# Optimization experiments

Hardware: AMD Instinct MI355X
Metric: run time of the kernel (lower is better)

Reference implementation:

```python
import jax, jax.numpy as jnp
import numpy as np

B, T, S, H, E, V, NUM_OOV = 32, 32, 100, 512, 300, 45000, 10
INF = 1e12


def setup_inputs() -> dict:
    key = jax.random.key(0)
    ks = jax.random.split(key, 24)
    def n(k, shape, s=0.02):
        return jax.random.normal(k, shape, jnp.float32) * s
    return dict(
        trg_seq=jax.random.randint(ks[0], (B, T), 0, V),
        ext_src_seq=jax.random.randint(ks[1], (B, S), 0, V + NUM_OOV),
        h0=n(ks[2], (1, B, H), 0.1),
        c0=n(ks[3], (1, B, H), 0.1),
        tree_output=n(ks[4], (B, S, H), 1.0),
        tree_enc_states=n(ks[5], (1, B, H), 0.1),
        encoder_outputs=n(ks[6], (B, S, H), 1.0),
        encoder_mask=jnp.zeros((B, S), bool),
        embedding=n(ks[7], (V, E)),
        W_enc=n(ks[8], (2 * H, H)), b_enc=jnp.zeros((H,), jnp.float32),
        W_red=n(ks[9], (E + H, E)), b_red=jnp.zeros((E,), jnp.float32),
        W_ih=n(ks[10], (E, 4 * H)), W_hh=n(ks[11], (H, 4 * H)),
        b_ih=jnp.zeros((4 * H,), jnp.float32), b_hh=jnp.zeros((4 * H,), jnp.float32),
        W_cat=n(ks[12], (2 * H, H)), b_cat=jnp.zeros((H,), jnp.float32),
        W_out=n(ks[13], (H, V)), b_out=jnp.zeros((V,), jnp.float32),
    )


def reference(trg_seq, ext_src_seq, h0, c0, tree_output, tree_enc_states,
              encoder_outputs, encoder_mask, embedding, W_enc, b_enc,
              W_red, b_red, W_ih, W_hh, b_ih, b_hh, W_cat, b_cat, W_out, b_out):
    # encoder features: [B,S,2H] -> [B,S,H]
    memories = jnp.concatenate([tree_output, encoder_outputs], axis=-1) @ W_enc + b_enc
    rows = jnp.arange(B)[:, None]  # for per-row scatter-max
    Vext = V + NUM_OOV

    def step(carry, y):
        h, c, ctx = carry  # h,c: [B,H], ctx: [B,H]
        emb = embedding[y]                                   # [B,E]
        x = jnp.concatenate([emb, ctx], axis=-1) @ W_red + b_red  # [B,E]
        gates = x @ W_ih + h @ W_hh + (b_ih + b_hh)          # [B,4H]
        i, f, g, o = jnp.split(gates, 4, axis=-1)            # torch gate order i,f,g,o
        c_new = jax.nn.sigmoid(f) * c + jax.nn.sigmoid(i) * jnp.tanh(g)
        h_new = jax.nn.sigmoid(o) * jnp.tanh(c_new)
        energy = jnp.einsum('bh,bsh->bs', h_new, memories)   # [B,S]
        energy = jnp.where(encoder_mask, -INF, energy)
        attn = jax.nn.softmax(energy, axis=-1)
        ctx_new = jnp.einsum('bs,bsh->bh', attn, memories)   # [B,H]
        z = jnp.tanh(jnp.concatenate([h_new, ctx_new], axis=-1) @ W_cat + b_cat)
        logit = z @ W_out + b_out                            # [B,V]
        # pointer copy mechanism: scatter-max of energies into extended vocab
        ext = jnp.concatenate([logit, jnp.zeros((B, NUM_OOV), logit.dtype)], axis=-1)
        scat = jnp.full((B, Vext), -INF, logit.dtype).at[rows, ext_src_seq].max(energy)
        scat = jnp.where(scat == -INF, 0.0, scat)
        out = ext + scat
        out = jnp.where(out == 0.0, -INF, out)
        return (h_new, c_new, ctx_new), out

    init = (h0[0], c0[0], jnp.zeros((B, H), memories.dtype))
    _, logits = jax.lax.scan(step, init, trg_seq.T)  # [T,B,Vext]
    return jnp.transpose(logits, (1, 0, 2))          # [B,T,Vext]
```

## Files before the change

### kernel.cpp

```cpp
#include <hip/hip_runtime.h>
#include <hip/hip_bf16.h>
#include <stdint.h>

typedef __hip_bfloat16 bf16;
typedef __attribute__((ext_vector_type(8))) short short8;
typedef __attribute__((ext_vector_type(4))) float f32x4;

#define INFV 1e12f

constexpr int Vv = 45000;
constexpr int VE = 45010;

static __device__ __forceinline__ float bf2f(unsigned short u){
  union{ unsigned int i; float f; } w; w.i = ((unsigned int)u) << 16; return w.f;
}
static __device__ __forceinline__ unsigned short f2bf(float x){
  union { __hip_bfloat16 h; unsigned short u; } w; w.h = __float2bfloat16(x); return w.u;
}

__launch_bounds__(256, 2)
__global__ void k_mm(const unsigned short* __restrict__ A, int lda,
                     const unsigned short* __restrict__ B, int ldb, int NB,
                     const float* __restrict__ bias,
                     void* __restrict__ C, int ldc,
                     int M, int N, int NZ, int K, int mode)
{
  __shared__ char smem[20480];
  char* smA = smem;
  char* smB = smem + 10240;
  int tid = threadIdx.x, lane = tid & 63;
  int w = tid >> 6, wr = w >> 1, wc = w & 1;
  int m0 = blockIdx.y * 128, n0 = blockIdx.x * 128;
  int l15 = lane & 15, lh = lane >> 4;
  f32x4 zero = {0.f,0.f,0.f,0.f};
  f32x4 acc[4][4];
  #pragma unroll
  for (int mi = 0; mi < 4; ++mi)
    #pragma unroll
    for (int ni = 0; ni < 4; ++ni) acc[mi][ni] = zero;
  short8 z8 = {0,0,0,0,0,0,0,0};

  for (int kc = 0; kc < K; kc += 32){
    #pragma unroll
    for (int call = 0; call < 2; ++call){
      int o = call*4096 + tid*16;
      int r = o >> 6, cb = o & 63;
      short8 va = z8, vb = z8;
      if (m0 + r < M)  va = *(const short8*)((const char*)A + ((size_t)(m0+r)*lda + kc)*2 + cb);
      if (n0 + r < NB) vb = *(const short8*)((const char*)B + ((size_t)(n0+r)*ldb + kc)*2 + cb);
      *(short8*)(smA + r*80 + cb) = va;
      *(short8*)(smB + r*80 + cb) = vb;
    }
    __syncthreads();
    short8 af[4], bfv[4];
    #pragma unroll
    for (int mi = 0; mi < 4; ++mi) af[mi]  = *(const short8*)(smA + (wr*64 + mi*16 + l15)*80 + lh*16);
    #pragma unroll
    for (int ni = 0; ni < 4; ++ni) bfv[ni] = *(const short8*)(smB + (wc*64 + ni*16 + l15)*80 + lh*16);
    #pragma unroll
    for (int mi = 0; mi < 4; ++mi)
      #pragma unroll
      for (int ni = 0; ni < 4; ++ni)
        acc[mi][ni] = __builtin_amdgcn_mfma_f32_16x16x32_bf16(af[mi], bfv[ni], acc[mi][ni], 0, 0, 0);
    __syncthreads();
  }

  #pragma unroll
  for (int mi = 0; mi < 4; ++mi){
    #pragma unroll
    for (int ni = 0; ni < 4; ++ni){
      #pragma unroll
      for (int j = 0; j < 4; ++j){
        int gr = m0 + wr*64 + mi*16 + 4*lh + j;
        int cg = n0 + wc*64 + ni*16 + l15;
        if (gr < M && cg < NZ){
          float v = (cg < N) ? acc[mi][ni][j] + (bias ? bias[cg] : 0.f) : 0.f;
          if (mode == 0) ((float*)C)[(size_t)gr*ldc + cg] = v;
          else {
            if (mode == 2) v = tanhf(v);
            ((unsigned short*)C)[(size_t)gr*ldc + cg] = f2bf(v);
          }
        }
      }
    }
  }
}

__launch_bounds__(256)
__global__ void k_tbf(const float* __restrict__ in, int ldin,
                      unsigned short* __restrict__ out,
                      int K, int N, int K2, int N2)
{
  __shared__ float tl[64][65];
  int n0 = blockIdx.x * 64, k0 = blockIdx.y * 64;
  int tid = threadIdx.x;
  for (int idx = tid; idx < 64*64; idx += 256){
    int r = idx >> 6, c = idx & 63;
    int gk = k0 + r, gn = n0 + c;
    tl[r][c] = (gk < K && gn < N) ? in[(size_t)gk*ldin + gn] : 0.f;
  }
  __syncthreads();
  for (int idx = tid; idx < 64*64; idx += 256){
    int r = idx >> 6, c = idx & 63;
    int gn = n0 + r, gk = k0 + c;
    if (gn < N2 && gk < K2) out[(size_t)gn*K2 + gk] = f2bf(tl[c][r]);
  }
}

__global__ void k_cat2bf(const float* __restrict__ tree, const float* __restrict__ enc,
                         unsigned short* __restrict__ Acat){
  int i = blockIdx.x*256 + threadIdx.x;
  if (i >= 3200*1024) return;
  int r = i >> 10, c = i & 1023;
  float v = (c < 512) ? tree[(size_t)r*512 + c] : enc[(size_t)r*512 + (c - 512)];
  Acat[i] = f2bf(v);
}

__global__ void k_gatherbf(const int* __restrict__ trg, const float* __restrict__ emb,
                           unsigned short* __restrict__ EmbAb){
  int i = blockIdx.x*256 + threadIdx.x;
  if (i >= 1024*320) return;
  int r = i / 320, c = i - r*320;
  EmbAb[i] = (c < 300) ? f2bf(emb[(size_t)trg[r]*300 + c]) : (unsigned short)0;
}

__global__ void k_cvtpad(const float* __restrict__ in, unsigned short* __restrict__ out){
  int i = blockIdx.x*256 + threadIdx.x;
  if (i >= 512*320) return;
  int r = i / 320, c = i - r*320;
  out[i] = (c < 300) ? f2bf(in[(size_t)r*300 + c]) : (unsigned short)0;
}

__global__ void k_bsum(const float* __restrict__ a, const float* __restrict__ b,
                       float* __restrict__ o){
  int i = blockIdx.x*256 + threadIdx.x;
  if (i < 2048) o[i] = a[i] + b[i];
}

__global__ void k_wgt(const float* __restrict__ Wf, const float* __restrict__ W_hh,
                      unsigned short* __restrict__ WgT){
  int idx = blockIdx.x*256 + threadIdx.x;
  if (idx >= 2048*1024) return;
  int cp = idx >> 10, k = idx & 1023;
  int c = (cp & 3)*512 + (cp >> 2);
  float v = (k < 512) ? Wf[(size_t)k*2048 + c] : W_hh[(size_t)(k-512)*2048 + c];
  WgT[idx] = f2bf(v);
}

__global__ void k_init(const float* __restrict__ h0, const float* __restrict__ c0,
                       unsigned short* __restrict__ HCa, float* __restrict__ Cst){
  int i = blockIdx.x*256 + threadIdx.x;
  if (i < 32*1024){
    int b = i >> 10, k = i & 1023;
    HCa[i] = (k < 512) ? f2bf(0.f) : f2bf(h0[b*512 + (k - 512)]);
  }
  if (i < 32*512) Cst[i] = c0[i];
}

__launch_bounds__(256, 1)
__global__ void k_gates(const unsigned short* __restrict__ WgT,
                        const unsigned short* __restrict__ HCprev,
                        unsigned short* __restrict__ HCnext,
                        float* __restrict__ C_state,
                        const float* __restrict__ G1,
                        unsigned short* __restrict__ HCz,
                        int t)
{
  __shared__ char Bsm[64*272];
  int tid = threadIdx.x;
  int lane = tid & 63, w2 = tid >> 6;
  int blk = blockIdx.x;
  int l15 = lane & 15, lh = lane >> 4;
  f32x4 zero = {0.f,0.f,0.f,0.f};
  f32x4 acc0 = zero, acc1 = zero;
  const char* Ab = (const char*)HCprev;

  for (int kc = 0; kc < 1024; kc += 128){
    #pragma unroll
    for (int call = 0; call < 4; ++call){
      int o = call*4096 + tid*16;
      int r = o >> 8, cb = o & 255;
      short8 v = *(const short8*)((const char*)WgT + (size_t)(blk*64 + r)*2048 + kc*2 + cb);
      *(short8*)(Bsm + r*272 + cb) = v;
    }
    __syncthreads();
    #pragma unroll
    for (int ks = 0; ks < 4; ++ks){
      short8 a0 = *(const short8*)(Ab + (size_t)l15*2048      + (kc + ks*32)*2 + lh*16);
      short8 a1 = *(const short8*)(Ab + (size_t)(l15+16)*2048 + (kc + ks*32)*2 + lh*16);
      int br = w2*16 + l15;
      short8 bfr = *(const short8*)(Bsm + br*272 + ks*64 + lh*16);
      acc0 = __builtin_amdgcn_mfma_f32_16x16x32_bf16(a0, bfr, acc0, 0, 0, 0);
      acc1 = __builtin_amdgcn_mfma_f32_16x16x32_bf16(a1, bfr, acc1, 0, 0, 0);
    }
    __syncthreads();
  }

  int cg = blk*64 + w2*16 + l15;
  int hfull = cg >> 2, q = cg & 3;
  #pragma unroll
  for (int f = 0; f < 2; ++f){
    #pragma unroll
    for (int j = 0; j < 4; ++j){
      int b = f*16 + 4*lh + j;
      float g = (f ? acc1[j] : acc0[j]) + G1[((size_t)b*32 + t)*2048 + q*512 + hfull];
      float x1 = (q == 2) ? tanhf(g) : 1.f/(1.f + expf(-g));
      float xg = __shfl_xor(x1, 2);
      float xf = __shfl_xor(x1, 1);
      float xo = __shfl_xor(x1, 3);
      if (q == 0){
        float co = C_state[b*512 + hfull];
        float cn = xf*co + x1*xg;
        float hn = xo * tanhf(cn);
        C_state[b*512 + hfull] = cn;
        unsigned short hb = f2bf(hn);
        HCnext[b*1024 + 512 + hfull] = hb;
        HCz[((size_t)b*32 + t)*1024 + hfull] = hb;
      }
    }
  }
}

__launch_bounds__(256, 1)
__global__ void k_attn(const unsigned short* __restrict__ memB,
                       const unsigned char* __restrict__ emask,
                       unsigned short* __restrict__ HCnext,
                       unsigned short* __restrict__ HCz,
                       float* __restrict__ Esave,
                       int t)
{
  int b = blockIdx.x;
  int tid = threadIdx.x, lane = tid & 63, w = tid >> 6;
  __shared__ float E_s[100];
  __shared__ float attn_s[100];
  float hreg[8];
  {
    short8 hv = *(const short8*)(HCnext + b*1024 + 512 + lane*8);
    #pragma unroll
    for (int i = 0; i < 8; ++i) hreg[i] = bf2f((unsigned short)hv[i]);
  }
  for (int s = w; s < 100; s += 4){
    short8 mv = *(const short8*)(memB + ((size_t)b*100 + s)*512 + lane*8);
    float a = 0.f;
    #pragma unroll
    for (int i = 0; i < 8; ++i) a = fmaf(hreg[i], bf2f((unsigned short)mv[i]), a);
    #pragma unroll
    for (int d = 1; d < 64; d <<= 1) a += __shfl_xor(a, d);
    if (lane == 0){
      float e = emask[b*100 + s] ? -INFV : a;
      E_s[s] = e;
      Esave[((size_t)b*32 + t)*100 + s] = e;
    }
  }
  __syncthreads();
  if (w == 0){
    float ea = (lane < 100) ? E_s[lane] : -INFV;
    float eb = (lane + 64 < 100) ? E_s[lane + 64] : -INFV;
    float m = fmaxf(ea, eb);
    #pragma unroll
    for (int d = 1; d < 64; d <<= 1) m = fmaxf(m, __shfl_xor(m, d));
    float p = ((lane < 100) ? expf(ea - m) : 0.f) + ((lane + 64 < 100) ? expf(eb - m) : 0.f);
    #pragma unroll
    for (int d = 1; d < 64; d <<= 1) p += __shfl_xor(p, d);
    float inv = 1.f / p;
    if (lane < 100)      attn_s[lane]      = expf(ea - m) * inv;
    if (lane + 64 < 100) attn_s[lane + 64] = expf(eb - m) * inv;
  }
  __syncthreads();
  for (int hh = tid; hh < 512; hh += 256){
    float a = 0.f;
    for (int s = 0; s < 100; ++s)
      a = fmaf(attn_s[s], bf2f(memB[((size_t)b*100 + s)*512 + hh]), a);
    unsigned short cbv = f2bf(a);
    HCnext[b*1024 + hh] = cbv;
    HCz[((size_t)b*32 + t)*1024 + 512 + hh] = cbv;
  }
}

__launch_bounds__(256, 4)
__global__ void k_logits(const unsigned short* __restrict__ Zbf,
                         const unsigned short* __restrict__ WoT,
                         const float* __restrict__ b_out,
                         const float* __restrict__ Esave,
                         const int* __restrict__ ext_src,
                         float* __restrict__ out)
{
  __shared__ char smem[32768];
  char* smA = smem;
  char* smB = smem + 10240;
  int tid = threadIdx.x, lane = tid & 63;
  int w = tid >> 6, wr = w >> 1, wc = w & 1;
  int m0 = blockIdx.y * 128, n0 = blockIdx.x * 128;
  int l15 = lane & 15, lh = lane >> 4;
  f32x4 zero = {0.f,0.f,0.f,0.f};
  f32x4 acc[4][4];
  #pragma unroll
  for (int mi = 0; mi < 4; ++mi)
    #pragma unroll
    for (int ni = 0; ni < 4; ++ni) acc[mi][ni] = zero;

  for (int kc = 0; kc < 512; kc += 32){
    #pragma unroll
    for (int call = 0; call < 2; ++call){
      int o = call*4096 + tid*16;
      int r = o >> 6, cb = o & 63;
      short8 va = *(const short8*)((const char*)Zbf + (size_t)(m0 + r)*1024 + kc*2 + cb);
      *(short8*)(smA + r*80 + cb) = va;
      short8 vb = *(const short8*)((const char*)WoT + (size_t)(n0 + r)*1024 + kc*2 + cb);
      *(short8*)(smB + r*80 + cb) = vb;
    }
    __syncthreads();
    short8 af[4], bfv[4];
    #pragma unroll
    for (int mi = 0; mi < 4; ++mi) af[mi]  = *(const short8*)(smA + (wr*64 + mi*16 + l15)*80 + lh*16);
    #pragma unroll
    for (int ni = 0; ni < 4; ++ni) bfv[ni] = *(const short8*)(smB + (wc*64 + ni*16 + l15)*80 + lh*16);
    #pragma unroll
    for (int mi = 0; mi < 4; ++mi)
      #pragma unroll
      for (int ni = 0; ni < 4; ++ni)
        acc[mi][ni] = __builtin_amdgcn_mfma_f32_16x16x32_bf16(af[mi], bfv[ni], acc[mi][ni], 0, 0, 0);
    __syncthreads();
  }

  float* smax = (float*)smem;
  for (int half = 0; half < 2; ++half){
    for (int i = tid; i < 64*128; i += 256) smax[i] = -INFV;
    __syncthreads();
    if (tid < 64){
      int rg = m0 + half*64 + tid;
      int b = rg >> 5;
      const int* es = ext_src + b*100;
      const float* ev = Esave + (size_t)rg*100;
      float* row = smax + tid*128;
      for (int s = 0; s < 100; ++s){
        unsigned int d = (unsigned int)(es[s] - n0);
        if (d < 128u){
          float e = ev[s];
          if (e > -9e11f && e > row[d]) row[d] = e;
        }
      }
    }
    __syncthreads();
    if (wr == half){
      #pragma unroll
      for (int mi = 0; mi < 4; ++mi){
        #pragma unroll
        for (int ni = 0; ni < 4; ++ni){
          #pragma unroll
          for (int j = 0; j < 4; ++j){
            int rll = mi*16 + 4*lh + j;
            int cl = wc*64 + ni*16 + l15;
            int cg = n0 + cl;
            if (cg < VE){
              float v = acc[mi][ni][j];
              float base = (cg < Vv) ? (v + b_out[cg]) : 0.f;
              float sm = smax[rll*128 + cl];
              float o = base + (sm > -9e11f ? sm : 0.f);
              if (o == 0.f) o = -INFV;
              out[(size_t)(m0 + half*64 + rll)*VE + cg] = o;
            }
          }
        }
      }
    }
    __syncthreads();
  }
}

extern "C" void kernel_launch(void* const* d_in, const int* in_sizes, int n_in,
                              void* d_out, int out_size, void* d_ws, size_t ws_size,
                              hipStream_t stream)
{
  const int*   trg    = (const int*)  d_in[0];
  const int*   ext    = (const int*)  d_in[1];
  const float* h0     = (const float*)d_in[2];
  const float* c0     = (const float*)d_in[3];
  const float* tree   = (const float*)d_in[4];
  const float* enc    = (const float*)d_in[6];
  const unsigned char* emask = (const unsigned char*)d_in[7];
  const float* emb    = (const float*)d_in[8];
  const float* W_enc  = (const float*)d_in[9];
  const float* b_enc  = (const float*)d_in[10];
  const float* W_red  = (const float*)d_in[11];
  const float* b_red  = (const float*)d_in[12];
  const float* W_ih   = (const float*)d_in[13];
  const float* W_hh   = (const float*)d_in[14];
  const float* b_ih   = (const float*)d_in[15];
  const float* b_hh   = (const float*)d_in[16];
  const float* W_cat  = (const float*)d_in[17];
  const float* b_cat  = (const float*)d_in[18];
  const float* W_out  = (const float*)d_in[19];
  const float* b_out  = (const float*)d_in[20];
  float* out = (float*)d_out;

  char* ws = (char*)d_ws;
  size_t off = 0;
  auto alloc = [&](size_t bytes)->char*{
    char* p = ws + off; off = (off + bytes + 255) & ~(size_t)255; return p;
  };
  unsigned short* Acat  = (unsigned short*)alloc(3200ull*1024*2);
  unsigned short* WencT = (unsigned short*)alloc(512ull*1024*2);
  unsigned short* memB  = (unsigned short*)alloc(3200ull*512*2);
  unsigned short* EmbAb = (unsigned short*)alloc(1024ull*320*2);
  unsigned short* WredT1= (unsigned short*)alloc(320ull*320*2);
  unsigned short* X0b   = (unsigned short*)alloc(1024ull*320*2);
  unsigned short* WihT  = (unsigned short*)alloc(2048ull*320*2);
  float*          G1    = (float*)         alloc(1024ull*2048*4);
  float*          bsum  = (float*)         alloc(2048*4);
  unsigned short* Wred2b= (unsigned short*)alloc(512ull*320*2);
  unsigned short* WgT   = (unsigned short*)alloc(2048ull*1024*2);
  unsigned short* WoT   = (unsigned short*)alloc(45056ull*512*2);
  unsigned short* WcatT = (unsigned short*)alloc(512ull*1024*2);
  unsigned short* HCa   = (unsigned short*)alloc(32*1024*2);
  unsigned short* HCb   = (unsigned short*)alloc(32*1024*2);
  float*          Cst   = (float*)         alloc(32*512*4);
  unsigned short* HCz   = (unsigned short*)alloc(1024ull*1024*2);
  unsigned short* Zbf   = (unsigned short*)alloc(1024ull*512*2);
  float*          Esave = (float*)         alloc(1024ull*100*4);
  float*          Wf    = (float*)Acat;

  k_cat2bf<<<12800, 256, 0, stream>>>(tree, enc, Acat);
  k_tbf<<<dim3(8,16), 256, 0, stream>>>(W_enc, 512, WencT, 1024, 512, 1024, 512);
  k_mm<<<dim3(4,25), 256, 0, stream>>>(Acat, 1024, WencT, 1024, 512, b_enc,
                                       memB, 512, 3200, 512, 512, 1024, 1);

  k_gatherbf<<<1280, 256, 0, stream>>>(trg, emb, EmbAb);
  k_tbf<<<dim3(5,5), 256, 0, stream>>>(W_red, 300, WredT1, 300, 300, 320, 320);
  k_tbf<<<dim3(32,5), 256, 0, stream>>>(W_ih, 2048, WihT, 300, 2048, 320, 2048);
  k_bsum<<<8, 256, 0, stream>>>(b_ih, b_hh, bsum);
  k_mm<<<dim3(3,8), 256, 0, stream>>>(EmbAb, 320, WredT1, 320, 320, b_red,
                                      X0b, 320, 1024, 300, 320, 320, 1);
  k_mm<<<dim3(16,8), 256, 0, stream>>>(X0b, 320, WihT, 320, 2048, bsum,
                                       G1, 2048, 1024, 2048, 2048, 320, 0);

  k_cvtpad<<<640, 256, 0, stream>>>(W_red + 300*300, Wred2b);
  k_mm<<<dim3(16,4), 256, 0, stream>>>(Wred2b, 320, WihT, 320, 2048, nullptr,
                                       Wf, 2048, 512, 2048, 2048, 320, 0);
  k_wgt<<<8192, 256, 0, stream>>>(Wf, W_hh, WgT);

  k_tbf<<<dim3(704,8), 256, 0, stream>>>(W_out, 45000, WoT, 512, 45000, 512, 45056);
  k_tbf<<<dim3(8,16), 256, 0, stream>>>(W_cat, 512, WcatT, 1024, 512, 1024, 512);
  k_init<<<128, 256, 0, stream>>>(h0, c0, HCa, Cst);

  for (int t = 0; t < 32; ++t){
    unsigned short* hp = (t & 1) ? HCb : HCa;
    unsigned short* hn = (t & 1) ? HCa : HCb;
    k_gates<<<32, 256, 0, stream>>>(WgT, hp, hn, Cst, G1, HCz, t);
    k_attn <<<32, 256, 0, stream>>>(memB, emask, hn, HCz, Esave, t);
  }

  k_mm<<<dim3(4,8), 256, 0, stream>>>(HCz, 1024, WcatT, 1024, 512, b_cat,
                                      Zbf, 512, 1024, 512, 512, 1024, 2);
  k_logits<<<dim3(352,8), 256, 0, stream>>>(Zbf, WoT, b_out, Esave, ext, out);
}
```

Measured before the change: 1.952 ms.

## Fuse recurrent loop into persistent kernel with grid barriers and LDS-resident weights

The 64 per-timestep gate and attention launches are replaced by a single persistent 64-block kernel. 32 blocks keep their slice of the combined gate weights in swizzled LDS and compute the LSTM gates; 32 blocks keep per-batch memories in LDS and compute attention. A software grid barrier separates the two phases of each step. Small preprocessing kernels are merged into two launches, and the context-projection GEMM is folded into the G1 GEMM by stacking inputs. The logits kernel also gains register prefetch and builds its scatter-max over all 128 rows in one pass. The intent is to remove launch overhead and repeated weight reloads; the cost is reliance on spin barriers, which assume all 64 blocks are co-resident.

```diff
diff --git a/kernel.cpp b/kernel.cpp
--- a/kernel.cpp
+++ b/kernel.cpp
@@ -86,14 +86,13 @@
   }
 }
 
-__launch_bounds__(256)
-__global__ void k_tbf(const float* __restrict__ in, int ldin,
-                      unsigned short* __restrict__ out,
-                      int K, int N, int K2, int N2)
+static __device__ __forceinline__ void tile64t(const float* __restrict__ in, int ldin,
+                                               unsigned short* __restrict__ out,
+                                               int K, int N, int K2, int N2,
+                                               int bx, int by, int tid)
 {
   __shared__ float tl[64][65];
-  int n0 = blockIdx.x * 64, k0 = blockIdx.y * 64;
-  int tid = threadIdx.x;
+  int n0 = bx * 64, k0 = by * 64;
   for (int idx = tid; idx < 64*64; idx += 256){
     int r = idx >> 6, c = idx & 63;
     int gk = k0 + r, gn = n0 + c;
@@ -107,177 +106,201 @@
   }
 }
 
-__global__ void k_cat2bf(const float* __restrict__ tree, const float* __restrict__ enc,
-                         unsigned short* __restrict__ Acat){
+__launch_bounds__(256)
+__global__ void k_trans(const float* __restrict__ W_out, unsigned short* __restrict__ WoT,
+                        const float* __restrict__ W_enc, unsigned short* __restrict__ WencT,
+                        const float* __restrict__ W_ih,  unsigned short* __restrict__ WihT,
+                        const float* __restrict__ W_red, unsigned short* __restrict__ WredT1,
+                        const float* __restrict__ W_cat, unsigned short* __restrict__ WcatT)
+{
+  int blk = blockIdx.x, tid = threadIdx.x;
+  if (blk < 5632)      tile64t(W_out, 45000, WoT,   512, 45000, 512, 45056, blk % 704,        blk / 704,        tid);
+  else if (blk < 5760) tile64t(W_enc, 512,   WencT, 1024, 512, 1024, 512,  (blk-5632) % 8,   (blk-5632) / 8,   tid);
+  else if (blk < 5920) tile64t(W_ih,  2048,  WihT,  300, 2048,  320, 2048, (blk-5760) % 32,  (blk-5760) / 32,  tid);
+  else if (blk < 5945) tile64t(W_red, 300,   WredT1,300, 300,   320, 320,  (blk-5920) % 5,   (blk-5920) / 5,   tid);
+  else                 tile64t(W_cat, 512,   WcatT, 1024, 512, 1024, 512,  (blk-5945) % 8,   (blk-5945) / 8,   tid);
+}
+
+__global__ void k_prep(const float* __restrict__ tree, const float* __restrict__ enc,
+                       unsigned short* __restrict__ Acat,
+                       const int* __restrict__ trg, const float* __restrict__ emb,
+                       unsigned short* __restrict__ EmbAb,
+                       const float* __restrict__ Wred2, unsigned short* __restrict__ Wred2b)
+{
   int i = blockIdx.x*256 + threadIdx.x;
-  if (i >= 3200*1024) return;
-  int r = i >> 10, c = i & 1023;
-  float v = (c < 512) ? tree[(size_t)r*512 + c] : enc[(size_t)r*512 + (c - 512)];
-  Acat[i] = f2bf(v);
-}
-
-__global__ void k_gatherbf(const int* __restrict__ trg, const float* __restrict__ emb,
-                           unsigned short* __restrict__ EmbAb){
-  int i = blockIdx.x*256 + threadIdx.x;
-  if (i >= 1024*320) return;
-  int r = i / 320, c = i - r*320;
-  EmbAb[i] = (c < 300) ? f2bf(emb[(size_t)trg[r]*300 + c]) : (unsigned short)0;
-}
-
-__global__ void k_cvtpad(const float* __restrict__ in, unsigned short* __restrict__ out){
-  int i = blockIdx.x*256 + threadIdx.x;
-  if (i >= 512*320) return;
-  int r = i / 320, c = i - r*320;
-  out[i] = (c < 300) ? f2bf(in[(size_t)r*300 + c]) : (unsigned short)0;
-}
-
-__global__ void k_bsum(const float* __restrict__ a, const float* __restrict__ b,
-                       float* __restrict__ o){
-  int i = blockIdx.x*256 + threadIdx.x;
-  if (i < 2048) o[i] = a[i] + b[i];
-}
-
-__global__ void k_wgt(const float* __restrict__ Wf, const float* __restrict__ W_hh,
-                      unsigned short* __restrict__ WgT){
-  int idx = blockIdx.x*256 + threadIdx.x;
-  if (idx >= 2048*1024) return;
-  int cp = idx >> 10, k = idx & 1023;
-  int c = (cp & 3)*512 + (cp >> 2);
-  float v = (k < 512) ? Wf[(size_t)k*2048 + c] : W_hh[(size_t)(k-512)*2048 + c];
-  WgT[idx] = f2bf(v);
-}
-
-__global__ void k_init(const float* __restrict__ h0, const float* __restrict__ c0,
-                       unsigned short* __restrict__ HCa, float* __restrict__ Cst){
-  int i = blockIdx.x*256 + threadIdx.x;
-  if (i < 32*1024){
-    int b = i >> 10, k = i & 1023;
-    HCa[i] = (k < 512) ? f2bf(0.f) : f2bf(h0[b*512 + (k - 512)]);
-  }
-  if (i < 32*512) Cst[i] = c0[i];
+  const int nA = 3200*1024, nB = 1024*320, nC = 512*320;
+  if (i < nA){
+    int r = i >> 10, c = i & 1023;
+    float v = (c < 512) ? tree[(size_t)r*512 + c] : enc[(size_t)r*512 + (c - 512)];
+    Acat[i] = f2bf(v);
+  } else if (i < nA + nB){
+    int i2 = i - nA;
+    int r = i2 / 320, c = i2 - r*320;
+    EmbAb[i2] = (c < 300) ? f2bf(emb[(size_t)trg[r]*300 + c]) : (unsigned short)0;
+  } else if (i < nA + nB + nC){
+    int i3 = i - nA - nB;
+    int r = i3 / 320, c = i3 - r*320;
+    Wred2b[i3] = (c < 300) ? f2bf(Wred2[(size_t)r*300 + c]) : (unsigned short)0;
+  }
+}
+
+static __device__ __forceinline__ void gbar(int* cnt, int* gen, int nblk){
+  __syncthreads();
+  if (threadIdx.x == 0){
+    __threadfence();
+    int g = __hip_atomic_load(gen, __ATOMIC_RELAXED, __HIP_MEMORY_SCOPE_AGENT);
+    int prev = __hip_atomic_fetch_add(cnt, 1, __ATOMIC_ACQ_REL, __HIP_MEMORY_SCOPE_AGENT);
+    if (prev == nblk - 1){
+      __hip_atomic_store(cnt, 0, __ATOMIC_RELAXED, __HIP_MEMORY_SCOPE_AGENT);
+      __hip_atomic_store(gen, g + 1, __ATOMIC_RELEASE, __HIP_MEMORY_SCOPE_AGENT);
+    } else {
+      while (__hip_atomic_load(gen, __ATOMIC_ACQUIRE, __HIP_MEMORY_SCOPE_AGENT) == g)
+        __builtin_amdgcn_s_sleep(2);
+    }
+    __threadfence();
+  }
+  __syncthreads();
 }
 
 __launch_bounds__(256, 1)
-__global__ void k_gates(const unsigned short* __restrict__ WgT,
-                        const unsigned short* __restrict__ HCprev,
-                        unsigned short* __restrict__ HCnext,
-                        float* __restrict__ C_state,
-                        const float* __restrict__ G1,
-                        unsigned short* __restrict__ HCz,
-                        int t)
-{
-  __shared__ char Bsm[64*272];
-  int tid = threadIdx.x;
-  int lane = tid & 63, w2 = tid >> 6;
-  int blk = blockIdx.x;
-  int l15 = lane & 15, lh = lane >> 4;
-  f32x4 zero = {0.f,0.f,0.f,0.f};
-  f32x4 acc0 = zero, acc1 = zero;
-  const char* Ab = (const char*)HCprev;
-
-  for (int kc = 0; kc < 1024; kc += 128){
-    #pragma unroll
-    for (int call = 0; call < 4; ++call){
-      int o = call*4096 + tid*16;
-      int r = o >> 8, cb = o & 255;
-      short8 v = *(const short8*)((const char*)WgT + (size_t)(blk*64 + r)*2048 + kc*2 + cb);
-      *(short8*)(Bsm + r*272 + cb) = v;
-    }
-    __syncthreads();
-    #pragma unroll
-    for (int ks = 0; ks < 4; ++ks){
-      short8 a0 = *(const short8*)(Ab + (size_t)l15*2048      + (kc + ks*32)*2 + lh*16);
-      short8 a1 = *(const short8*)(Ab + (size_t)(l15+16)*2048 + (kc + ks*32)*2 + lh*16);
-      int br = w2*16 + l15;
-      short8 bfr = *(const short8*)(Bsm + br*272 + ks*64 + lh*16);
-      acc0 = __builtin_amdgcn_mfma_f32_16x16x32_bf16(a0, bfr, acc0, 0, 0, 0);
-      acc1 = __builtin_amdgcn_mfma_f32_16x16x32_bf16(a1, bfr, acc1, 0, 0, 0);
-    }
-    __syncthreads();
-  }
-
-  int cg = blk*64 + w2*16 + l15;
-  int hfull = cg >> 2, q = cg & 3;
-  #pragma unroll
-  for (int f = 0; f < 2; ++f){
-    #pragma unroll
-    for (int j = 0; j < 4; ++j){
-      int b = f*16 + 4*lh + j;
-      float g = (f ? acc1[j] : acc0[j]) + G1[((size_t)b*32 + t)*2048 + q*512 + hfull];
-      float x1 = (q == 2) ? tanhf(g) : 1.f/(1.f + expf(-g));
-      float xg = __shfl_xor(x1, 2);
-      float xf = __shfl_xor(x1, 1);
-      float xo = __shfl_xor(x1, 3);
-      if (q == 0){
-        float co = C_state[b*512 + hfull];
-        float cn = xf*co + x1*xg;
-        float hn = xo * tanhf(cn);
-        C_state[b*512 + hfull] = cn;
-        unsigned short hb = f2bf(hn);
-        HCnext[b*1024 + 512 + hfull] = hb;
-        HCz[((size_t)b*32 + t)*1024 + hfull] = hb;
-      }
-    }
-  }
-}
-
-__launch_bounds__(256, 1)
-__global__ void k_attn(const unsigned short* __restrict__ memB,
-                       const unsigned char* __restrict__ emask,
-                       unsigned short* __restrict__ HCnext,
-                       unsigned short* __restrict__ HCz,
-                       float* __restrict__ Esave,
-                       int t)
-{
-  int b = blockIdx.x;
-  int tid = threadIdx.x, lane = tid & 63, w = tid >> 6;
-  __shared__ float E_s[100];
-  __shared__ float attn_s[100];
-  float hreg[8];
-  {
-    short8 hv = *(const short8*)(HCnext + b*1024 + 512 + lane*8);
-    #pragma unroll
-    for (int i = 0; i < 8; ++i) hreg[i] = bf2f((unsigned short)hv[i]);
-  }
-  for (int s = w; s < 100; s += 4){
-    short8 mv = *(const short8*)(memB + ((size_t)b*100 + s)*512 + lane*8);
-    float a = 0.f;
-    #pragma unroll
-    for (int i = 0; i < 8; ++i) a = fmaf(hreg[i], bf2f((unsigned short)mv[i]), a);
-    #pragma unroll
-    for (int d = 1; d < 64; d <<= 1) a += __shfl_xor(a, d);
-    if (lane == 0){
-      float e = emask[b*100 + s] ? -INFV : a;
-      E_s[s] = e;
-      Esave[((size_t)b*32 + t)*100 + s] = e;
-    }
-  }
-  __syncthreads();
-  if (w == 0){
-    float ea = (lane < 100) ? E_s[lane] : -INFV;
-    float eb = (lane + 64 < 100) ? E_s[lane + 64] : -INFV;
-    float m = fmaxf(ea, eb);
-    #pragma unroll
-    for (int d = 1; d < 64; d <<= 1) m = fmaxf(m, __shfl_xor(m, d));
-    float p = ((lane < 100) ? expf(ea - m) : 0.f) + ((lane + 64 < 100) ? expf(eb - m) : 0.f);
-    #pragma unroll
-    for (int d = 1; d < 64; d <<= 1) p += __shfl_xor(p, d);
-    float inv = 1.f / p;
-    if (lane < 100)      attn_s[lane]      = expf(ea - m) * inv;
-    if (lane + 64 < 100) attn_s[lane + 64] = expf(eb - m) * inv;
-  }
-  __syncthreads();
-  for (int hh = tid; hh < 512; hh += 256){
-    float a = 0.f;
-    for (int s = 0; s < 100; ++s)
-      a = fmaf(attn_s[s], bf2f(memB[((size_t)b*100 + s)*512 + hh]), a);
-    unsigned short cbv = f2bf(a);
-    HCnext[b*1024 + hh] = cbv;
-    HCz[((size_t)b*32 + t)*1024 + 512 + hh] = cbv;
-  }
-}
-
-__launch_bounds__(256, 4)
+__global__ void k_rec(const float* __restrict__ Wf, const float* __restrict__ W_hh,
+                      const float* __restrict__ G1,
+                      const float* __restrict__ b_ih, const float* __restrict__ b_hh,
+                      const float* __restrict__ h0, const float* __restrict__ c0,
+                      const unsigned short* __restrict__ memB,
+                      const unsigned char* __restrict__ emask,
+                      unsigned short* __restrict__ HCa, unsigned short* __restrict__ HCb,
+                      unsigned short* __restrict__ HCz, float* __restrict__ Esave,
+                      int* __restrict__ bar)
+{
+  __shared__ char lds[131072];
+  int tid = threadIdx.x, lane = tid & 63, blk = blockIdx.x;
+  int* cnt = bar; int* gen = bar + 16;
+
+  if (blk < 32){
+    int w2 = tid >> 6, l15 = lane & 15, lh = lane >> 4;
+    for (int it = 0; it < 256; ++it){
+      int grp = it*16 + (tid >> 4);
+      int k = grp >> 2, q = grp & 3, i = tid & 15;
+      int cl = 4*i + q;
+      float v = (k < 512) ? Wf  [(size_t)k      *2048 + q*512 + blk*16 + i]
+                          : W_hh[(size_t)(k-512)*2048 + q*512 + blk*16 + i];
+      *(unsigned short*)(lds + cl*2048 + ((k*2) ^ ((cl & 7) << 4))) = f2bf(v);
+    }
+    int cg = blk*64 + w2*16 + l15;
+    int hfull = cg >> 2, q = cg & 3;
+    float bsumv = b_ih[q*512 + hfull] + b_hh[q*512 + hfull];
+    float creg[2][4];
+    #pragma unroll
+    for (int f = 0; f < 2; ++f)
+      #pragma unroll
+      for (int j = 0; j < 4; ++j)
+        creg[f][j] = c0[(f*16 + 4*lh + j)*512 + hfull];
+
+    gbar(cnt, gen, 64);
+
+    for (int t = 0; t < 32; ++t){
+      const char* Ab = (const char*)((t & 1) ? HCb : HCa);
+      unsigned short* HCn = (t & 1) ? HCa : HCb;
+      f32x4 zero = {0.f,0.f,0.f,0.f};
+      f32x4 acc0 = zero, acc1 = zero;
+      int cl = w2*16 + l15;
+      int xm = (cl & 7) << 4;
+      #pragma unroll 8
+      for (int kc = 0; kc < 1024; kc += 32){
+        short8 a0 = *(const short8*)(Ab + l15*2048      + kc*2 + lh*16);
+        short8 a1 = *(const short8*)(Ab + (l15+16)*2048 + kc*2 + lh*16);
+        short8 bfr = *(const short8*)(lds + cl*2048 + ((kc*2 + lh*16) ^ xm));
+        acc0 = __builtin_amdgcn_mfma_f32_16x16x32_bf16(a0, bfr, acc0, 0, 0, 0);
+        acc1 = __builtin_amdgcn_mfma_f32_16x16x32_bf16(a1, bfr, acc1, 0, 0, 0);
+      }
+      #pragma unroll
+      for (int f = 0; f < 2; ++f){
+        #pragma unroll
+        for (int j = 0; j < 4; ++j){
+          int brow = f*16 + 4*lh + j;
+          float g = (f ? acc1[j] : acc0[j])
+                  + G1[((size_t)brow*32 + t)*2048 + q*512 + hfull] + bsumv;
+          float x1 = (q == 2) ? tanhf(g) : 1.f/(1.f + expf(-g));
+          float xg = __shfl_xor(x1, 2);
+          float xf = __shfl_xor(x1, 1);
+          float xo = __shfl_xor(x1, 3);
+          if (q == 0){
+            float cn = xf*creg[f][j] + x1*xg;
+            creg[f][j] = cn;
+            float hn = xo * tanhf(cn);
+            unsigned short hb = f2bf(hn);
+            HCn[brow*1024 + 512 + hfull] = hb;
+            HCz[((size_t)brow*32 + t)*1024 + hfull] = hb;
+          }
+        }
+      }
+      gbar(cnt, gen, 64);
+      gbar(cnt, gen, 64);
+    }
+  } else {
+    int b = blk - 32;
+    float* E_s   = (float*)(lds + 102400);
+    float* att_s = (float*)(lds + 102816);
+    for (int idx = tid; idx < 6400; idx += 256)
+      *(short8*)(lds + idx*16) = *(const short8*)((const char*)memB + (size_t)b*102400 + idx*16);
+    for (int i = tid; i < 1024; i += 256)
+      HCa[b*1024 + i] = (i < 512) ? (unsigned short)0 : f2bf(h0[b*512 + i - 512]);
+
+    gbar(cnt, gen, 64);
+
+    int w = tid >> 6;
+    for (int t = 0; t < 32; ++t){
+      gbar(cnt, gen, 64);
+      unsigned short* HCn = (t & 1) ? HCa : HCb;
+      float hreg[8];
+      {
+        short8 hv = *(const short8*)(HCn + b*1024 + 512 + lane*8);
+        #pragma unroll
+        for (int i = 0; i < 8; ++i) hreg[i] = bf2f((unsigned short)hv[i]);
+      }
+      for (int s = w; s < 100; s += 4){
+        short8 mv = *(const short8*)(lds + s*1024 + lane*16);
+        float a = 0.f;
+        #pragma unroll
+        for (int i = 0; i < 8; ++i) a = fmaf(hreg[i], bf2f((unsigned short)mv[i]), a);
+        #pragma unroll
+        for (int d = 1; d < 64; d <<= 1) a += __shfl_xor(a, d);
+        if (lane == 0){
+          float e = emask[b*100 + s] ? -INFV : a;
+          E_s[s] = e;
+          Esave[((size_t)b*32 + t)*100 + s] = e;
+        }
+      }
+      __syncthreads();
+      if (w == 0){
+        float ea = (lane < 100) ? E_s[lane] : -INFV;
+        float eb = (lane + 64 < 100) ? E_s[lane + 64] : -INFV;
+        float m = fmaxf(ea, eb);
+        #pragma unroll
+        for (int d = 1; d < 64; d <<= 1) m = fmaxf(m, __shfl_xor(m, d));
+        float p = ((lane < 100) ? expf(ea - m) : 0.f) + ((lane + 64 < 100) ? expf(eb - m) : 0.f);
+        #pragma unroll
+        for (int d = 1; d < 64; d <<= 1) p += __shfl_xor(p, d);
+        float inv = 1.f / p;
+        if (lane < 100)      att_s[lane]      = expf(ea - m) * inv;
+        if (lane + 64 < 100) att_s[lane + 64] = expf(eb - m) * inv;
+      }
+      __syncthreads();
+      for (int hh = tid; hh < 512; hh += 256){
+        float a = 0.f;
+        for (int s = 0; s < 100; ++s)
+          a = fmaf(att_s[s], bf2f(*(const unsigned short*)(lds + s*1024 + hh*2)), a);
+        unsigned short cbv = f2bf(a);
+        HCn[b*1024 + hh] = cbv;
+        HCz[((size_t)b*32 + t)*1024 + 512 + hh] = cbv;
+      }
+      gbar(cnt, gen, 64);
+    }
+  }
+}
+
+__launch_bounds__(256, 2)
 __global__ void k_logits(const unsigned short* __restrict__ Zbf,
                          const unsigned short* __restrict__ WoT,
                          const float* __restrict__ b_out,
@@ -285,7 +308,7 @@
                          const int* __restrict__ ext_src,
                          float* __restrict__ out)
 {
-  __shared__ char smem[32768];
+  __shared__ char smem[65536];
   char* smA = smem;
   char* smB = smem + 10240;
   int tid = threadIdx.x, lane = tid & 63;
@@ -299,17 +322,29 @@
     #pragma unroll
     for (int ni = 0; ni < 4; ++ni) acc[mi][ni] = zero;
 
+  short8 va[2], vb[2];
+  #pragma unroll
+  for (int call = 0; call < 2; ++call){
+    int o = call*4096 + tid*16; int r = o >> 6, cb = o & 63;
+    va[call] = *(const short8*)((const char*)Zbf + (size_t)(m0 + r)*1024 + cb);
+    vb[call] = *(const short8*)((const char*)WoT + (size_t)(n0 + r)*1024 + cb);
+  }
   for (int kc = 0; kc < 512; kc += 32){
     #pragma unroll
     for (int call = 0; call < 2; ++call){
-      int o = call*4096 + tid*16;
-      int r = o >> 6, cb = o & 63;
-      short8 va = *(const short8*)((const char*)Zbf + (size_t)(m0 + r)*1024 + kc*2 + cb);
-      *(short8*)(smA + r*80 + cb) = va;
-      short8 vb = *(const short8*)((const char*)WoT + (size_t)(n0 + r)*1024 + kc*2 + cb);
-      *(short8*)(smB + r*80 + cb) = vb;
+      int o = call*4096 + tid*16; int r = o >> 6, cb = o & 63;
+      *(short8*)(smA + r*80 + cb) = va[call];
+      *(short8*)(smB + r*80 + cb) = vb[call];
     }
     __syncthreads();
+    if (kc < 480){
+      #pragma unroll
+      for (int call = 0; call < 2; ++call){
+        int o = call*4096 + tid*16; int r = o >> 6, cb = o & 63;
+        va[call] = *(const short8*)((const char*)Zbf + (size_t)(m0 + r)*1024 + (kc+32)*2 + cb);
+        vb[call] = *(const short8*)((const char*)WoT + (size_t)(n0 + r)*1024 + (kc+32)*2 + cb);
+      }
+    }
     short8 af[4], bfv[4];
     #pragma unroll
     for (int mi = 0; mi < 4; ++mi) af[mi]  = *(const short8*)(smA + (wr*64 + mi*16 + l15)*80 + lh*16);
@@ -324,47 +359,43 @@
   }
 
   float* smax = (float*)smem;
-  for (int half = 0; half < 2; ++half){
-    for (int i = tid; i < 64*128; i += 256) smax[i] = -INFV;
-    __syncthreads();
-    if (tid < 64){
-      int rg = m0 + half*64 + tid;
-      int b = rg >> 5;
-      const int* es = ext_src + b*100;
-      const float* ev = Esave + (size_t)rg*100;
-      float* row = smax + tid*128;
-      for (int s = 0; s < 100; ++s){
-        unsigned int d = (unsigned int)(es[s] - n0);
-        if (d < 128u){
-          float e = ev[s];
-          if (e > -9e11f && e > row[d]) row[d] = e;
+  for (int i = tid; i < 128*128; i += 256) smax[i] = -INFV;
+  __syncthreads();
+  if (tid < 128){
+    int rg = m0 + tid;
+    int b = rg >> 5;
+    const int* es = ext_src + b*100;
+    const float* ev = Esave + (size_t)rg*100;
+    float* row = smax + tid*128;
+    for (int s = 0; s < 100; ++s){
+      unsigned int d = (unsigned int)(es[s] - n0);
+      if (d < 128u){
+        float e = ev[s];
+        if (e > -9e11f && e > row[d]) row[d] = e;
+      }
+    }
+  }
+  __syncthreads();
+
+  #pragma unroll
+  for (int mi = 0; mi < 4; ++mi){
+    #pragma unroll
+    for (int ni = 0; ni < 4; ++ni){
+      #pragma unroll
+      for (int j = 0; j < 4; ++j){
+        int rl = wr*64 + mi*16 + 4*lh + j;
+        int cl = wc*64 + ni*16 + l15;
+        int cg = n0 + cl;
+        if (cg < VE){
+          float v = acc[mi][ni][j];
+          float base = (cg < Vv) ? (v + b_out[cg]) : 0.f;
+          float sm = smax[rl*128 + cl];
+          float o = base + (sm > -9e11f ? sm : 0.f);
+          if (o == 0.f) o = -INFV;
+          out[(size_t)(m0 + rl)*VE + cg] = o;
         }
       }
     }
-    __syncthreads();
-    if (wr == half){
-      #pragma unroll
-      for (int mi = 0; mi < 4; ++mi){
-        #pragma unroll
-        for (int ni = 0; ni < 4; ++ni){
-          #pragma unroll
-          for (int j = 0; j < 4; ++j){
-            int rll = mi*16 + 4*lh + j;
-            int cl = wc*64 + ni*16 + l15;
-            int cg = n0 + cl;
-            if (cg < VE){
-              float v = acc[mi][ni][j];
-              float base = (cg < Vv) ? (v + b_out[cg]) : 0.f;
-              float sm = smax[rll*128 + cl];
-              float o = base + (sm > -9e11f ? sm : 0.f);
-              if (o == 0.f) o = -INFV;
-              out[(size_t)(m0 + half*64 + rll)*VE + cg] = o;
-            }
-          }
-        }
-      }
-    }
-    __syncthreads();
   }
 }
 
@@ -405,50 +436,36 @@
   unsigned short* EmbAb = (unsigned short*)alloc(1024ull*320*2);
   unsigned short* WredT1= (unsigned short*)alloc(320ull*320*2);
   unsigned short* X0b   = (unsigned short*)alloc(1024ull*320*2);
+  unsigned short* Wred2b= (unsigned short*)alloc(512ull*320*2);
   unsigned short* WihT  = (unsigned short*)alloc(2048ull*320*2);
   float*          G1    = (float*)         alloc(1024ull*2048*4);
-  float*          bsum  = (float*)         alloc(2048*4);
-  unsigned short* Wred2b= (unsigned short*)alloc(512ull*320*2);
-  unsigned short* WgT   = (unsigned short*)alloc(2048ull*1024*2);
+  float*          Wfbuf = (float*)         alloc(512ull*2048*4);
   unsigned short* WoT   = (unsigned short*)alloc(45056ull*512*2);
   unsigned short* WcatT = (unsigned short*)alloc(512ull*1024*2);
   unsigned short* HCa   = (unsigned short*)alloc(32*1024*2);
   unsigned short* HCb   = (unsigned short*)alloc(32*1024*2);
-  float*          Cst   = (float*)         alloc(32*512*4);
   unsigned short* HCz   = (unsigned short*)alloc(1024ull*1024*2);
   unsigned short* Zbf   = (unsigned short*)alloc(1024ull*512*2);
   float*          Esave = (float*)         alloc(1024ull*100*4);
-  float*          Wf    = (float*)Acat;
-
-  k_cat2bf<<<12800, 256, 0, stream>>>(tree, enc, Acat);
-  k_tbf<<<dim3(8,16), 256, 0, stream>>>(W_enc, 512, WencT, 1024, 512, 1024, 512);
+  int*            bar   = (int*)           alloc(256);
+  (void)Wred2b; (void)Wfbuf;
+
+  hipMemsetAsync(bar, 0, 128, stream);
+
+  k_trans<<<6073, 256, 0, stream>>>(W_out, WoT, W_enc, WencT, W_ih, WihT,
+                                    W_red, WredT1, W_cat, WcatT);
+  k_prep<<<14720, 256, 0, stream>>>(tree, enc, Acat, trg, emb, EmbAb,
+                                    W_red + 300*300, Wred2b);
+
   k_mm<<<dim3(4,25), 256, 0, stream>>>(Acat, 1024, WencT, 1024, 512, b_enc,
                                        memB, 512, 3200, 512, 512, 1024, 1);
-
-  k_gatherbf<<<1280, 256, 0, stream>>>(trg, emb, EmbAb);
-  k_tbf<<<dim3(5,5), 256, 0, stream>>>(W_red, 300, WredT1, 300, 300, 320, 320);
-  k_tbf<<<dim3(32,5), 256, 0, stream>>>(W_ih, 2048, WihT, 300, 2048, 320, 2048);
-  k_bsum<<<8, 256, 0, stream>>>(b_ih, b_hh, bsum);
   k_mm<<<dim3(3,8), 256, 0, stream>>>(EmbAb, 320, WredT1, 320, 320, b_red,
                                       X0b, 320, 1024, 300, 320, 320, 1);
-  k_mm<<<dim3(16,8), 256, 0, stream>>>(X0b, 320, WihT, 320, 2048, bsum,
-                                       G1, 2048, 1024, 2048, 2048, 320, 0);
-
-  k_cvtpad<<<640, 256, 0, stream>>>(W_red + 300*300, Wred2b);
-  k_mm<<<dim3(16,4), 256, 0, stream>>>(Wred2b, 320, WihT, 320, 2048, nullptr,
-                                       Wf, 2048, 512, 2048, 2048, 320, 0);
-  k_wgt<<<8192, 256, 0, stream>>>(Wf, W_hh, WgT);
-
-  k_tbf<<<dim3(704,8), 256, 0, stream>>>(W_out, 45000, WoT, 512, 45000, 512, 45056);
-  k_tbf<<<dim3(8,16), 256, 0, stream>>>(W_cat, 512, WcatT, 1024, 512, 1024, 512);
-  k_init<<<128, 256, 0, stream>>>(h0, c0, HCa, Cst);
-
-  for (int t = 0; t < 32; ++t){
-    unsigned short* hp = (t & 1) ? HCb : HCa;
-    unsigned short* hn = (t & 1) ? HCa : HCb;
-    k_gates<<<32, 256, 0, stream>>>(WgT, hp, hn, Cst, G1, HCz, t);
-    k_attn <<<32, 256, 0, stream>>>(memB, emask, hn, HCz, Esave, t);
-  }
+  k_mm<<<dim3(16,12), 256, 0, stream>>>(X0b, 320, WihT, 320, 2048, nullptr,
+                                        G1, 2048, 1536, 2048, 2048, 320, 0);
+
+  k_rec<<<64, 256, 0, stream>>>(G1 + 1024ull*2048, W_hh, G1, b_ih, b_hh, h0, c0,
+                                memB, emask, HCa, HCb, HCz, Esave, bar);
 
   k_mm<<<dim3(4,8), 256, 0, stream>>>(HCz, 1024, WcatT, 1024, 512, b_cat,
                                       Zbf, 512, 1024, 512, 512, 1024, 2);
```

Result: slower. 2.011 ms (+3.1%).
